# Kernel tuning notes

Measured on AMD Instinct MI355X. Metric: run time of the kernel, lower is better.

## Reference

```python
import jax, jax.numpy as jnp
import numpy as np

TOP_K = 2


def setup_inputs() -> dict:
    key = jax.random.key(0)
    ks = jax.random.split(key, 5)
    T, D, F, E = 1024, 1024, 2048, 16
    scale_d = 1.0 / np.sqrt(D)
    scale_f = 1.0 / np.sqrt(F)
    return {
        "x_TD": jax.random.normal(ks[0], (T, D), jnp.float32),
        "router_w_DE": jax.random.normal(ks[1], (D, E), jnp.float32) * scale_d,
        "kernel_gating_EDF": jax.random.normal(ks[2], (E, D, F), jnp.float32) * scale_d,
        "kernel_up_EDF": jax.random.normal(ks[3], (E, D, F), jnp.float32) * scale_d,
        "kernel_down_EFD": jax.random.normal(ks[4], (E, F, D), jnp.float32) * scale_f,
    }


def _router(x_TD, router_w_DE):
    # linear router -> softmax -> top-k, renormalized weights
    logits_TE = x_TD @ router_w_DE
    probs_TE = jax.nn.softmax(logits_TE, axis=-1)
    weights_TX, indices_TX = jax.lax.top_k(probs_TE, TOP_K)
    weights_TX = weights_TX / jnp.sum(weights_TX, axis=-1, keepdims=True)
    return weights_TX, indices_TX


def reference(x_TD, router_w_DE, kernel_gating_EDF, kernel_up_EDF, kernel_down_EFD):
    E = kernel_gating_EDF.shape[0]
    weights_TX, indices_TX = _router(x_TD, router_w_DE)
    # scatter top-k weights into a dense (T, E) combine matrix via one-hot
    one_hot_TXE = jax.nn.one_hot(indices_TX, E, dtype=x_TD.dtype)
    full_weights_TE = jnp.sum(one_hot_TXE * weights_TX[..., None], axis=1)
    # dense all-experts MoE (as in _moe_fwd)
    gating_TEF = jnp.einsum("TD,EDF->TEF", x_TD, kernel_gating_EDF)
    up_TEF = jnp.einsum("TD,EDF->TEF", x_TD, kernel_up_EDF)
    fuse_TEF = jax.nn.silu(gating_TEF) * up_TEF
    down_TED = jnp.einsum("TEF,EFD->TED", fuse_TEF, kernel_down_EFD)
    out_TD = jnp.einsum("TED,TE->TD", down_TED, full_weights_TE)
    return out_TD.astype(x_TD.dtype)
```

## Files before the change

kernel.cpp:

```cpp
#include <hip/hip_runtime.h>
#include <hip/hip_bf16.h>

typedef __bf16 bf16_t;
typedef __bf16 bf16x8 __attribute__((ext_vector_type(8)));
typedef __bf16 bf16x4 __attribute__((ext_vector_type(4)));
typedef float  f32x4  __attribute__((ext_vector_type(4)));

#define T_TOK 1024
#define DDIM  1024
#define FDIM  2048
#define NEXP  16
#define MAXR  192

#define WS_ENTRY_OFF   1024
#define WS_ENTRYW_OFF  66560
#define WS_XG_OFF      132096
#define WS_PART_OFF    132096
#define WS_FUSE_OFF    8520704

#define GLL16(g, l) __builtin_amdgcn_global_load_lds(                      \
    (const __attribute__((address_space(1))) unsigned int*)(g),            \
    (__attribute__((address_space(3))) unsigned int*)(l), 16, 0, 0)

#define FENCE()   asm volatile("" ::: "memory")
#define WAITVM(N) asm volatile("s_waitcnt vmcnt(" #N ")" ::: "memory")
#define WAITLG()  asm volatile("s_waitcnt lgkmcnt(0)" ::: "memory")
#define SCHEDB()  __builtin_amdgcn_sched_barrier(0)
#define SBAR()    __builtin_amdgcn_s_barrier()

__global__ __launch_bounds__(64) void router_kernel(
    const float* __restrict__ x, const float* __restrict__ rw,
    int* __restrict__ cnt, int* __restrict__ entry, float* __restrict__ entry_w)
{
    const int t = blockIdx.x;
    const int lane = threadIdx.x;
    float acc[NEXP];
#pragma unroll
    for (int e = 0; e < NEXP; ++e) acc[e] = 0.f;
#pragma unroll
    for (int i = 0; i < DDIM / 64; ++i) {
        const int d = lane + i * 64;
        const float xv = x[(size_t)t * DDIM + d];
        const float* r = rw + (size_t)d * NEXP;
#pragma unroll
        for (int e = 0; e < NEXP; ++e) acc[e] += xv * r[e];
    }
#pragma unroll
    for (int e = 0; e < NEXP; ++e) {
        float v = acc[e];
        for (int off = 32; off > 0; off >>= 1) v += __shfl_down(v, off);
        acc[e] = v;
    }
    if (lane == 0) {
        int i0 = -1, i1 = -1;
        float v0 = -1e30f, v1 = -1e30f;
#pragma unroll
        for (int e = 0; e < NEXP; ++e) {
            const float v = acc[e];
            if (v > v0)      { v1 = v0; i1 = i0; v0 = v; i0 = e; }
            else if (v > v1) { v1 = v;  i1 = e; }
        }
        const float e1 = __expf(v1 - v0);
        const float w0 = 1.f / (1.f + e1);
        const float w1 = e1 / (1.f + e1);
        int p = atomicAdd(&cnt[i0], 1);
        entry[i0 * T_TOK + p] = t * 2 + 0;
        entry_w[i0 * T_TOK + p] = w0;
        p = atomicAdd(&cnt[i1], 1);
        entry[i1 * T_TOK + p] = t * 2 + 1;
        entry_w[i1 * T_TOK + p] = w1;
    }
}

__global__ __launch_bounds__(256) void gather_kernel(
    const float* __restrict__ x, const int* __restrict__ cnt,
    const int* __restrict__ entry, bf16_t* __restrict__ xg)
{
    const int e  = blockIdx.x;
    const int i0 = blockIdx.y * 4;
    const int tid = threadIdx.x;
    int n_tok = cnt[e]; if (n_tok > MAXR) n_tok = MAXR;
#pragma unroll
    for (int rr = 0; rr < 4; ++rr) {
        const int i = i0 + rr;
        bf16x4 v4;
        v4[0] = (bf16_t)0.f; v4[1] = (bf16_t)0.f; v4[2] = (bf16_t)0.f; v4[3] = (bf16_t)0.f;
        if (i < n_tok) {
            const int tok = entry[e * T_TOK + i] >> 1;
            const float4 v = *(const float4*)(x + (size_t)tok * DDIM + tid * 4);
            v4[0] = (bf16_t)v.x; v4[1] = (bf16_t)v.y; v4[2] = (bf16_t)v.z; v4[3] = (bf16_t)v.w;
        }
        *(bf16x4*)(xg + ((size_t)e * MAXR + i) * DDIM + tid * 4) = v4;
    }
}

__global__ __launch_bounds__(256, 2) void ffn1_kernel(
    const bf16_t* __restrict__ xg,
    const float* __restrict__ wg, const float* __restrict__ wu,
    const int* __restrict__ cnt, const int* __restrict__ entry,
    bf16_t* __restrict__ fuse)
{
    const int e  = blockIdx.x;
    const int f0 = blockIdx.y * 64;
    int n_tok = cnt[e]; if (n_tok > MAXR) n_tok = MAXR;

    __shared__ __align__(16) bf16_t As[2][MAXR][32];
    __shared__ __align__(16) bf16_t Bgs[2][64][40];
    __shared__ __align__(16) bf16_t Bus[2][64][40];
    __shared__ int sem[MAXR];

    const int tid  = threadIdx.x;
    const int wave = tid >> 6;
    const int lane = tid & 63;
    const int r    = lane & 15;
    const int q    = lane >> 4;
    const int arow = lane >> 2;
    const int slot = (lane & 3) ^ (arow & 3);

    const bf16_t* xg_e = xg + (size_t)e * MAXR * DDIM;
    const float* wg_p = wg + (size_t)e * DDIM * FDIM + (size_t)(wave * 8) * FDIM + f0 + lane;
    const float* wu_p = wu + (size_t)e * DDIM * FDIM + (size_t)(wave * 8) * FDIM + f0 + lane;

    if (tid < MAXR) sem[tid] = (tid < n_tok) ? entry[e * T_TOK + tid] : -1;

    float rg[8], ru[8];
#pragma unroll
    for (int j = 0; j < 8; ++j) { rg[j] = wg_p[(size_t)j * FDIM]; ru[j] = wu_p[(size_t)j * FDIM]; }
    FENCE();
#pragma unroll
    for (int c = 0; c < 3; ++c) {
        const int rowb = wave * 48 + c * 16;
        const bf16_t* g = xg_e + (size_t)(rowb + arow) * DDIM + slot * 8;
        GLL16(g, &As[0][rowb][0] + lane * 8);
    }
    FENCE();
    WAITVM(3);
    {
        bf16x8 pg, pu;
#pragma unroll
        for (int j = 0; j < 8; ++j) { pg[j] = (bf16_t)rg[j]; pu[j] = (bf16_t)ru[j]; }
        *(bf16x8*)&Bgs[0][lane][wave * 8] = pg;
        *(bf16x8*)&Bus[0][lane][wave * 8] = pu;
    }
    wg_p += (size_t)32 * FDIM; wu_p += (size_t)32 * FDIM;
#pragma unroll
    for (int j = 0; j < 8; ++j) { rg[j] = wg_p[(size_t)j * FDIM]; ru[j] = wu_p[(size_t)j * FDIM]; }
    FENCE();
#pragma unroll
    for (int c = 0; c < 3; ++c) {
        const int rowb = wave * 48 + c * 16;
        const bf16_t* g = xg_e + (size_t)(rowb + arow) * DDIM + 32 + slot * 8;
        GLL16(g, &As[1][rowb][0] + lane * 8);
    }
    FENCE();
    WAITLG();
    SBAR();

    f32x4 accg[3][4], accu[3][4];
#pragma unroll
    for (int a = 0; a < 3; ++a)
#pragma unroll
        for (int b = 0; b < 4; ++b) {
            accg[a][b] = (f32x4){0.f, 0.f, 0.f, 0.f};
            accu[a][b] = (f32x4){0.f, 0.f, 0.f, 0.f};
        }

    for (int t = 0; t < 32; ++t) {
        const int cur = t & 1;
        if (t == 31) { WAITVM(0); } else { WAITVM(19); }
        SCHEDB();
        bf16x8 af[3], bg[4], bu[4];
#pragma unroll
        for (int mt = 0; mt < 3; ++mt) {
            const int m = wave * 48 + mt * 16 + r;
            af[mt] = *(const bf16x8*)&As[cur][m][(q ^ (r & 3)) * 8];
        }
#pragma unroll
        for (int nt = 0; nt < 4; ++nt) {
            bg[nt] = *(const bf16x8*)&Bgs[cur][nt * 16 + r][q * 8];
            bu[nt] = *(const bf16x8*)&Bus[cur][nt * 16 + r][q * 8];
        }
        if (t < 31) {
            WAITVM(3);
            bf16x8 pg, pu;
#pragma unroll
            for (int j = 0; j < 8; ++j) { pg[j] = (bf16_t)rg[j]; pu[j] = (bf16_t)ru[j]; }
            *(bf16x8*)&Bgs[cur ^ 1][lane][wave * 8] = pg;
            *(bf16x8*)&Bus[cur ^ 1][lane][wave * 8] = pu;
        }
        WAITLG();
        SCHEDB();
        if (t < 30) {
            wg_p += (size_t)32 * FDIM; wu_p += (size_t)32 * FDIM;
#pragma unroll
            for (int j = 0; j < 8; ++j) { rg[j] = wg_p[(size_t)j * FDIM]; ru[j] = wu_p[(size_t)j * FDIM]; }
            FENCE();
            const int kk = (t + 2) * 32;
#pragma unroll
            for (int c = 0; c < 3; ++c) {
                const int rowb = wave * 48 + c * 16;
                const bf16_t* g = xg_e + (size_t)(rowb + arow) * DDIM + kk + slot * 8;
                GLL16(g, &As[cur][rowb][0] + lane * 8);
            }
            FENCE();
        }
        __builtin_amdgcn_s_setprio(1);
#pragma unroll
        for (int mt = 0; mt < 3; ++mt)
#pragma unroll
            for (int nt = 0; nt < 4; ++nt) {
                accg[mt][nt] = __builtin_amdgcn_mfma_f32_16x16x32_bf16(af[mt], bg[nt], accg[mt][nt], 0, 0, 0);
                accu[mt][nt] = __builtin_amdgcn_mfma_f32_16x16x32_bf16(af[mt], bu[nt], accu[mt][nt], 0, 0, 0);
            }
        __builtin_amdgcn_s_setprio(0);
        SBAR();
    }

    bf16_t* fuse_e = fuse + (size_t)e * MAXR * FDIM + f0;
#pragma unroll
    for (int mt = 0; mt < 3; ++mt) {
#pragma unroll
        for (int j = 0; j < 4; ++j) {
            const int m = wave * 48 + mt * 16 + q * 4 + j;
            const bool valid = sem[m] >= 0;
            bf16_t* dst = fuse_e + (size_t)m * FDIM;
#pragma unroll
            for (int nt = 0; nt < 4; ++nt) {
                const float g = accg[mt][nt][j];
                const float u = accu[mt][nt][j];
                const float h = valid ? (g / (1.f + __expf(-g))) * u : 0.f;
                dst[nt * 16 + r] = (bf16_t)h;
            }
        }
    }
}

__global__ __launch_bounds__(256, 2) void ffn2_kernel(
    const bf16_t* __restrict__ fuse, const float* __restrict__ wd,
    const int* __restrict__ cnt, const int* __restrict__ entry,
    const float* __restrict__ entry_w, float* __restrict__ partial)
{
    const int e  = blockIdx.x;
    const int d0 = blockIdx.y * 32;
    int n_tok = cnt[e]; if (n_tok > MAXR) n_tok = MAXR;

    __shared__ __align__(16) bf16_t As[2][2][MAXR][32];
    __shared__ __align__(16) bf16_t Bs[2][32][72];
    __shared__ int   sem[MAXR];
    __shared__ float sw[MAXR];

    const int tid  = threadIdx.x;
    const int wave = tid >> 6;
    const int lane = tid & 63;
    const int r    = lane & 15;
    const int q    = lane >> 4;
    const int arow = lane >> 2;
    const int slot = (lane & 3) ^ (arow & 3);

    const bf16_t* fu_e = fuse + (size_t)e * MAXR * FDIM;
    const int bn = tid & 31;
    const int k8 = (tid >> 5) * 8;
    const float* wd_p = wd + (size_t)e * FDIM * DDIM + (size_t)k8 * DDIM + d0 + bn;

    if (tid < MAXR) {
        sem[tid] = (tid < n_tok) ? entry[e * T_TOK + tid] : -1;
        sw[tid]  = (tid < n_tok) ? entry_w[e * T_TOK + tid] : 0.f;
    }

    float rb[8];
#pragma unroll
    for (int j = 0; j < 8; ++j) rb[j] = wd_p[(size_t)j * DDIM];
    FENCE();
#pragma unroll
    for (int ks = 0; ks < 2; ++ks)
#pragma unroll
        for (int c = 0; c < 3; ++c) {
            const int rowb = wave * 48 + c * 16;
            const bf16_t* g = fu_e + (size_t)(rowb + arow) * FDIM + ks * 32 + slot * 8;
            GLL16(g, &As[0][ks][rowb][0] + lane * 8);
        }
    FENCE();
    WAITVM(6);
    {
        bf16x8 pb;
#pragma unroll
        for (int j = 0; j < 8; ++j) pb[j] = (bf16_t)rb[j];
        *(bf16x8*)&Bs[0][bn][k8] = pb;
    }
    wd_p += (size_t)64 * DDIM;
#pragma unroll
    for (int j = 0; j < 8; ++j) rb[j] = wd_p[(size_t)j * DDIM];
    FENCE();
#pragma unroll
    for (int ks = 0; ks < 2; ++ks)
#pragma unroll
        for (int c = 0; c < 3; ++c) {
            const int rowb = wave * 48 + c * 16;
            const bf16_t* g = fu_e + (size_t)(rowb + arow) * FDIM + 64 + ks * 32 + slot * 8;
            GLL16(g, &As[1][ks][rowb][0] + lane * 8);
        }
    FENCE();
    WAITLG();
    SBAR();

    f32x4 acc[3][2];
#pragma unroll
    for (int a = 0; a < 3; ++a)
#pragma unroll
        for (int b = 0; b < 2; ++b) acc[a][b] = (f32x4){0.f, 0.f, 0.f, 0.f};

    for (int t = 0; t < 32; ++t) {
        const int cur = t & 1;
        if (t == 31) { WAITVM(0); } else { WAITVM(14); }
        SCHEDB();
        bf16x8 af2[2][3], bb2[2][2];
#pragma unroll
        for (int ks = 0; ks < 2; ++ks) {
#pragma unroll
            for (int mt = 0; mt < 3; ++mt) {
                const int m = wave * 48 + mt * 16 + r;
                af2[ks][mt] = *(const bf16x8*)&As[cur][ks][m][(q ^ (r & 3)) * 8];
            }
#pragma unroll
            for (int nt = 0; nt < 2; ++nt)
                bb2[ks][nt] = *(const bf16x8*)&Bs[cur][nt * 16 + r][ks * 32 + q * 8];
        }
        if (t < 31) {
            WAITVM(6);
            bf16x8 pb;
#pragma unroll
            for (int j = 0; j < 8; ++j) pb[j] = (bf16_t)rb[j];
            *(bf16x8*)&Bs[cur ^ 1][bn][k8] = pb;
        }
        WAITLG();
        SCHEDB();
        if (t < 30) {
            wd_p += (size_t)64 * DDIM;
#pragma unroll
            for (int j = 0; j < 8; ++j) rb[j] = wd_p[(size_t)j * DDIM];
            FENCE();
            const int kk = (t + 2) * 64;
#pragma unroll
            for (int ks = 0; ks < 2; ++ks)
#pragma unroll
                for (int c = 0; c < 3; ++c) {
                    const int rowb = wave * 48 + c * 16;
                    const bf16_t* g = fu_e + (size_t)(rowb + arow) * FDIM + kk + ks * 32 + slot * 8;
                    GLL16(g, &As[cur][ks][rowb][0] + lane * 8);
                }
            FENCE();
        }
        __builtin_amdgcn_s_setprio(1);
#pragma unroll
        for (int ks = 0; ks < 2; ++ks)
#pragma unroll
            for (int mt = 0; mt < 3; ++mt)
#pragma unroll
                for (int nt = 0; nt < 2; ++nt)
                    acc[mt][nt] = __builtin_amdgcn_mfma_f32_16x16x32_bf16(af2[ks][mt], bb2[ks][nt], acc[mt][nt], 0, 0, 0);
        __builtin_amdgcn_s_setprio(0);
        SBAR();
    }

#pragma unroll
    for (int mt = 0; mt < 3; ++mt) {
#pragma unroll
        for (int j = 0; j < 4; ++j) {
            const int m = wave * 48 + mt * 16 + q * 4 + j;
            const int em = sem[m];
            if (em < 0) continue;
            const int t = em >> 1;
            const int sl = em & 1;
            const float w = sw[m];
            float* dst = partial + ((size_t)sl * T_TOK + t) * DDIM + d0;
#pragma unroll
            for (int nt = 0; nt < 2; ++nt)
                dst[nt * 16 + r] = acc[mt][nt][j] * w;
        }
    }
}

__global__ __launch_bounds__(256) void add_kernel(
    const float* __restrict__ partial, float* __restrict__ out)
{
    const int i = blockIdx.x * blockDim.x + threadIdx.x;
    const float4 a = ((const float4*)partial)[i];
    const float4 b = ((const float4*)(partial + (size_t)T_TOK * DDIM))[i];
    float4 o;
    o.x = a.x + b.x; o.y = a.y + b.y; o.z = a.z + b.z; o.w = a.w + b.w;
    ((float4*)out)[i] = o;
}

extern "C" void kernel_launch(void* const* d_in, const int* in_sizes, int n_in,
                              void* d_out, int out_size, void* d_ws, size_t ws_size,
                              hipStream_t stream) {
    const float* x  = (const float*)d_in[0];
    const float* rw = (const float*)d_in[1];
    const float* wg = (const float*)d_in[2];
    const float* wu = (const float*)d_in[3];
    const float* wd = (const float*)d_in[4];
    float* out = (float*)d_out;

    char* ws = (char*)d_ws;
    int*    cnt     = (int*)ws;
    int*    entry   = (int*)(ws + WS_ENTRY_OFF);
    float*  entry_w = (float*)(ws + WS_ENTRYW_OFF);
    bf16_t* xg      = (bf16_t*)(ws + WS_XG_OFF);
    float*  partial = (float*)(ws + WS_PART_OFF);
    bf16_t* fuse    = (bf16_t*)(ws + WS_FUSE_OFF);

    hipMemsetAsync(cnt, 0, 64, stream);

    router_kernel<<<T_TOK, 64, 0, stream>>>(x, rw, cnt, entry, entry_w);

    gather_kernel<<<dim3(NEXP, MAXR / 4), 256, 0, stream>>>(x, cnt, entry, xg);

    ffn1_kernel<<<dim3(NEXP, FDIM / 64), 256, 0, stream>>>(
        xg, wg, wu, cnt, entry, fuse);

    ffn2_kernel<<<dim3(NEXP, DDIM / 32), 256, 0, stream>>>(
        fuse, wd, cnt, entry, entry_w, partial);

    add_kernel<<<(T_TOK * DDIM / 4) / 256, 256, 0, stream>>>(partial, out);
}
```

Before: 432.5 us.

## Halve FFN tile widths for more blocks and stage router weights in LDS

```diff
diff --git a/kernel.cpp b/kernel.cpp
--- a/kernel.cpp
+++ b/kernel.cpp
@@ -4,6 +4,7 @@
 typedef __bf16 bf16_t;
 typedef __bf16 bf16x8 __attribute__((ext_vector_type(8)));
 typedef __bf16 bf16x4 __attribute__((ext_vector_type(4)));
+typedef __bf16 bf16x2 __attribute__((ext_vector_type(2)));
 typedef float  f32x4  __attribute__((ext_vector_type(4)));
 
 #define T_TOK 1024
@@ -28,22 +29,45 @@
 #define SCHEDB()  __builtin_amdgcn_sched_barrier(0)
 #define SBAR()    __builtin_amdgcn_s_barrier()
 
-__global__ __launch_bounds__(64) void router_kernel(
+__global__ __launch_bounds__(256) void router_kernel(
     const float* __restrict__ x, const float* __restrict__ rw,
     int* __restrict__ cnt, int* __restrict__ entry, float* __restrict__ entry_w)
 {
-    const int t = blockIdx.x;
-    const int lane = threadIdx.x;
+    __shared__ float rws[256][20];
+    const int tid  = threadIdx.x;
+    const int wave = tid >> 6;
+    const int lane = tid & 63;
+    const int t    = blockIdx.x * 4 + wave;
+
     float acc[NEXP];
 #pragma unroll
     for (int e = 0; e < NEXP; ++e) acc[e] = 0.f;
-#pragma unroll
-    for (int i = 0; i < DDIM / 64; ++i) {
-        const int d = lane + i * 64;
-        const float xv = x[(size_t)t * DDIM + d];
-        const float* r = rw + (size_t)d * NEXP;
-#pragma unroll
-        for (int e = 0; e < NEXP; ++e) acc[e] += xv * r[e];
+
+    for (int tile = 0; tile < 4; ++tile) {
+        const int d0 = tile * 256;
+        {
+            const float4* src = (const float4*)(rw + (size_t)(d0 + tid) * NEXP);
+            float4 a = src[0], b = src[1], c = src[2], d = src[3];
+            *(float4*)&rws[tid][0]  = a;
+            *(float4*)&rws[tid][4]  = b;
+            *(float4*)&rws[tid][8]  = c;
+            *(float4*)&rws[tid][12] = d;
+        }
+        __syncthreads();
+#pragma unroll
+        for (int i = 0; i < 4; ++i) {
+            const int row = i * 64 + lane;
+            const float xv = x[(size_t)t * DDIM + d0 + row];
+#pragma unroll
+            for (int e4 = 0; e4 < 4; ++e4) {
+                const float4 rv = *(const float4*)&rws[row][e4 * 4];
+                acc[e4 * 4 + 0] += xv * rv.x;
+                acc[e4 * 4 + 1] += xv * rv.y;
+                acc[e4 * 4 + 2] += xv * rv.z;
+                acc[e4 * 4 + 3] += xv * rv.w;
+            }
+        }
+        __syncthreads();
     }
 #pragma unroll
     for (int e = 0; e < NEXP; ++e) {
@@ -94,19 +118,19 @@
     }
 }
 
-__global__ __launch_bounds__(256, 2) void ffn1_kernel(
+__global__ __launch_bounds__(256, 4) void ffn1_kernel(
     const bf16_t* __restrict__ xg,
     const float* __restrict__ wg, const float* __restrict__ wu,
     const int* __restrict__ cnt, const int* __restrict__ entry,
     bf16_t* __restrict__ fuse)
 {
     const int e  = blockIdx.x;
-    const int f0 = blockIdx.y * 64;
+    const int f0 = blockIdx.y * 32;
     int n_tok = cnt[e]; if (n_tok > MAXR) n_tok = MAXR;
 
     __shared__ __align__(16) bf16_t As[2][MAXR][32];
-    __shared__ __align__(16) bf16_t Bgs[2][64][40];
-    __shared__ __align__(16) bf16_t Bus[2][64][40];
+    __shared__ __align__(16) bf16_t Bgs[2][32][40];
+    __shared__ __align__(16) bf16_t Bus[2][32][40];
     __shared__ int sem[MAXR];
 
     const int tid  = threadIdx.x;
@@ -116,16 +140,18 @@
     const int q    = lane >> 4;
     const int arow = lane >> 2;
     const int slot = (lane & 3) ^ (arow & 3);
+    const int bcol = lane & 31;
+    const int brow0 = wave * 8 + ((lane >> 5) << 2);
 
     const bf16_t* xg_e = xg + (size_t)e * MAXR * DDIM;
-    const float* wg_p = wg + (size_t)e * DDIM * FDIM + (size_t)(wave * 8) * FDIM + f0 + lane;
-    const float* wu_p = wu + (size_t)e * DDIM * FDIM + (size_t)(wave * 8) * FDIM + f0 + lane;
+    const float* wg_p = wg + (size_t)e * DDIM * FDIM + (size_t)brow0 * FDIM + f0 + bcol;
+    const float* wu_p = wu + (size_t)e * DDIM * FDIM + (size_t)brow0 * FDIM + f0 + bcol;
 
     if (tid < MAXR) sem[tid] = (tid < n_tok) ? entry[e * T_TOK + tid] : -1;
 
-    float rg[8], ru[8];
-#pragma unroll
-    for (int j = 0; j < 8; ++j) { rg[j] = wg_p[(size_t)j * FDIM]; ru[j] = wu_p[(size_t)j * FDIM]; }
+    float rg[4], ru[4];
+#pragma unroll
+    for (int j = 0; j < 4; ++j) { rg[j] = wg_p[(size_t)j * FDIM]; ru[j] = wu_p[(size_t)j * FDIM]; }
     FENCE();
 #pragma unroll
     for (int c = 0; c < 3; ++c) {
@@ -136,15 +162,15 @@
     FENCE();
     WAITVM(3);
     {
-        bf16x8 pg, pu;
-#pragma unroll
-        for (int j = 0; j < 8; ++j) { pg[j] = (bf16_t)rg[j]; pu[j] = (bf16_t)ru[j]; }
-        *(bf16x8*)&Bgs[0][lane][wave * 8] = pg;
-        *(bf16x8*)&Bus[0][lane][wave * 8] = pu;
+        bf16x4 pg, pu;
+#pragma unroll
+        for (int j = 0; j < 4; ++j) { pg[j] = (bf16_t)rg[j]; pu[j] = (bf16_t)ru[j]; }
+        *(bf16x4*)&Bgs[0][bcol][brow0] = pg;
+        *(bf16x4*)&Bus[0][bcol][brow0] = pu;
     }
     wg_p += (size_t)32 * FDIM; wu_p += (size_t)32 * FDIM;
 #pragma unroll
-    for (int j = 0; j < 8; ++j) { rg[j] = wg_p[(size_t)j * FDIM]; ru[j] = wu_p[(size_t)j * FDIM]; }
+    for (int j = 0; j < 4; ++j) { rg[j] = wg_p[(size_t)j * FDIM]; ru[j] = wu_p[(size_t)j * FDIM]; }
     FENCE();
 #pragma unroll
     for (int c = 0; c < 3; ++c) {
@@ -156,44 +182,44 @@
     WAITLG();
     SBAR();
 
-    f32x4 accg[3][4], accu[3][4];
+    f32x4 accg[3][2], accu[3][2];
 #pragma unroll
     for (int a = 0; a < 3; ++a)
 #pragma unroll
-        for (int b = 0; b < 4; ++b) {
+        for (int b = 0; b < 2; ++b) {
             accg[a][b] = (f32x4){0.f, 0.f, 0.f, 0.f};
             accu[a][b] = (f32x4){0.f, 0.f, 0.f, 0.f};
         }
 
     for (int t = 0; t < 32; ++t) {
         const int cur = t & 1;
-        if (t == 31) { WAITVM(0); } else { WAITVM(19); }
+        if (t == 31) { WAITVM(0); } else { WAITVM(11); }
         SCHEDB();
-        bf16x8 af[3], bg[4], bu[4];
+        bf16x8 af[3], bg[2], bu[2];
 #pragma unroll
         for (int mt = 0; mt < 3; ++mt) {
             const int m = wave * 48 + mt * 16 + r;
             af[mt] = *(const bf16x8*)&As[cur][m][(q ^ (r & 3)) * 8];
         }
 #pragma unroll
-        for (int nt = 0; nt < 4; ++nt) {
+        for (int nt = 0; nt < 2; ++nt) {
             bg[nt] = *(const bf16x8*)&Bgs[cur][nt * 16 + r][q * 8];
             bu[nt] = *(const bf16x8*)&Bus[cur][nt * 16 + r][q * 8];
         }
         if (t < 31) {
             WAITVM(3);
-            bf16x8 pg, pu;
-#pragma unroll
-            for (int j = 0; j < 8; ++j) { pg[j] = (bf16_t)rg[j]; pu[j] = (bf16_t)ru[j]; }
-            *(bf16x8*)&Bgs[cur ^ 1][lane][wave * 8] = pg;
-            *(bf16x8*)&Bus[cur ^ 1][lane][wave * 8] = pu;
+            bf16x4 pg, pu;
+#pragma unroll
+            for (int j = 0; j < 4; ++j) { pg[j] = (bf16_t)rg[j]; pu[j] = (bf16_t)ru[j]; }
+            *(bf16x4*)&Bgs[cur ^ 1][bcol][brow0] = pg;
+            *(bf16x4*)&Bus[cur ^ 1][bcol][brow0] = pu;
         }
         WAITLG();
         SCHEDB();
         if (t < 30) {
             wg_p += (size_t)32 * FDIM; wu_p += (size_t)32 * FDIM;
 #pragma unroll
-            for (int j = 0; j < 8; ++j) { rg[j] = wg_p[(size_t)j * FDIM]; ru[j] = wu_p[(size_t)j * FDIM]; }
+            for (int j = 0; j < 4; ++j) { rg[j] = wg_p[(size_t)j * FDIM]; ru[j] = wu_p[(size_t)j * FDIM]; }
             FENCE();
             const int kk = (t + 2) * 32;
 #pragma unroll
@@ -208,7 +234,7 @@
 #pragma unroll
         for (int mt = 0; mt < 3; ++mt)
 #pragma unroll
-            for (int nt = 0; nt < 4; ++nt) {
+            for (int nt = 0; nt < 2; ++nt) {
                 accg[mt][nt] = __builtin_amdgcn_mfma_f32_16x16x32_bf16(af[mt], bg[nt], accg[mt][nt], 0, 0, 0);
                 accu[mt][nt] = __builtin_amdgcn_mfma_f32_16x16x32_bf16(af[mt], bu[nt], accu[mt][nt], 0, 0, 0);
             }
@@ -225,7 +251,7 @@
             const bool valid = sem[m] >= 0;
             bf16_t* dst = fuse_e + (size_t)m * FDIM;
 #pragma unroll
-            for (int nt = 0; nt < 4; ++nt) {
+            for (int nt = 0; nt < 2; ++nt) {
                 const float g = accg[mt][nt][j];
                 const float u = accu[mt][nt][j];
                 const float h = valid ? (g / (1.f + __expf(-g))) * u : 0.f;
@@ -235,17 +261,17 @@
     }
 }
 
-__global__ __launch_bounds__(256, 2) void ffn2_kernel(
+__global__ __launch_bounds__(256, 4) void ffn2_kernel(
     const bf16_t* __restrict__ fuse, const float* __restrict__ wd,
     const int* __restrict__ cnt, const int* __restrict__ entry,
     const float* __restrict__ entry_w, float* __restrict__ partial)
 {
     const int e  = blockIdx.x;
-    const int d0 = blockIdx.y * 32;
+    const int d0 = blockIdx.y * 16;
     int n_tok = cnt[e]; if (n_tok > MAXR) n_tok = MAXR;
 
-    __shared__ __align__(16) bf16_t As[2][2][MAXR][32];
-    __shared__ __align__(16) bf16_t Bs[2][32][72];
+    __shared__ __align__(16) bf16_t As[2][MAXR][32];
+    __shared__ __align__(16) bf16_t Bs[2][16][40];
     __shared__ int   sem[MAXR];
     __shared__ float sw[MAXR];
 
@@ -256,108 +282,89 @@
     const int q    = lane >> 4;
     const int arow = lane >> 2;
     const int slot = (lane & 3) ^ (arow & 3);
+    const int bcol = lane & 15;
+    const int brow0 = wave * 8 + ((lane >> 4) << 1);
 
     const bf16_t* fu_e = fuse + (size_t)e * MAXR * FDIM;
-    const int bn = tid & 31;
-    const int k8 = (tid >> 5) * 8;
-    const float* wd_p = wd + (size_t)e * FDIM * DDIM + (size_t)k8 * DDIM + d0 + bn;
+    const float* wd_p = wd + (size_t)e * FDIM * DDIM + (size_t)brow0 * DDIM + d0 + bcol;
 
     if (tid < MAXR) {
         sem[tid] = (tid < n_tok) ? entry[e * T_TOK + tid] : -1;
         sw[tid]  = (tid < n_tok) ? entry_w[e * T_TOK + tid] : 0.f;
     }
 
-    float rb[8];
-#pragma unroll
-    for (int j = 0; j < 8; ++j) rb[j] = wd_p[(size_t)j * DDIM];
-    FENCE();
-#pragma unroll
-    for (int ks = 0; ks < 2; ++ks)
-#pragma unroll
-        for (int c = 0; c < 3; ++c) {
-            const int rowb = wave * 48 + c * 16;
-            const bf16_t* g = fu_e + (size_t)(rowb + arow) * FDIM + ks * 32 + slot * 8;
-            GLL16(g, &As[0][ks][rowb][0] + lane * 8);
-        }
-    FENCE();
-    WAITVM(6);
+    float rb[2];
+#pragma unroll
+    for (int j = 0; j < 2; ++j) rb[j] = wd_p[(size_t)j * DDIM];
+    FENCE();
+#pragma unroll
+    for (int c = 0; c < 3; ++c) {
+        const int rowb = wave * 48 + c * 16;
+        const bf16_t* g = fu_e + (size_t)(rowb + arow) * FDIM + slot * 8;
+        GLL16(g, &As[0][rowb][0] + lane * 8);
+    }
+    FENCE();
+    WAITVM(3);
     {
-        bf16x8 pb;
-#pragma unroll
-        for (int j = 0; j < 8; ++j) pb[j] = (bf16_t)rb[j];
-        *(bf16x8*)&Bs[0][bn][k8] = pb;
-    }
-    wd_p += (size_t)64 * DDIM;
-#pragma unroll
-    for (int j = 0; j < 8; ++j) rb[j] = wd_p[(size_t)j * DDIM];
-    FENCE();
-#pragma unroll
-    for (int ks = 0; ks < 2; ++ks)
-#pragma unroll
-        for (int c = 0; c < 3; ++c) {
-            const int rowb = wave * 48 + c * 16;
-            const bf16_t* g = fu_e + (size_t)(rowb + arow) * FDIM + 64 + ks * 32 + slot * 8;
-            GLL16(g, &As[1][ks][rowb][0] + lane * 8);
-        }
+        bf16x2 pb;
+        pb[0] = (bf16_t)rb[0]; pb[1] = (bf16_t)rb[1];
+        *(bf16x2*)&Bs[0][bcol][brow0] = pb;
+    }
+    wd_p += (size_t)32 * DDIM;
+#pragma unroll
+    for (int j = 0; j < 2; ++j) rb[j] = wd_p[(size_t)j * DDIM];
+    FENCE();
+#pragma unroll
+    for (int c = 0; c < 3; ++c) {
+        const int rowb = wave * 48 + c * 16;
+        const bf16_t* g = fu_e + (size_t)(rowb + arow) * FDIM + 32 + slot * 8;
+        GLL16(g, &As[1][rowb][0] + lane * 8);
+    }
     FENCE();
     WAITLG();
     SBAR();
 
-    f32x4 acc[3][2];
-#pragma unroll
-    for (int a = 0; a < 3; ++a)
-#pragma unroll
-        for (int b = 0; b < 2; ++b) acc[a][b] = (f32x4){0.f, 0.f, 0.f, 0.f};
-
-    for (int t = 0; t < 32; ++t) {
+    f32x4 acc[3];
+#pragma unroll
+    for (int a = 0; a < 3; ++a) acc[a] = (f32x4){0.f, 0.f, 0.f, 0.f};
+
+    for (int t = 0; t < 64; ++t) {
         const int cur = t & 1;
-        if (t == 31) { WAITVM(0); } else { WAITVM(14); }
+        if (t == 63) { WAITVM(0); } else { WAITVM(5); }
         SCHEDB();
-        bf16x8 af2[2][3], bb2[2][2];
-#pragma unroll
-        for (int ks = 0; ks < 2; ++ks) {
-#pragma unroll
-            for (int mt = 0; mt < 3; ++mt) {
-                const int m = wave * 48 + mt * 16 + r;
-                af2[ks][mt] = *(const bf16x8*)&As[cur][ks][m][(q ^ (r & 3)) * 8];
-            }
-#pragma unroll
-            for (int nt = 0; nt < 2; ++nt)
-                bb2[ks][nt] = *(const bf16x8*)&Bs[cur][nt * 16 + r][ks * 32 + q * 8];
-        }
-        if (t < 31) {
-            WAITVM(6);
-            bf16x8 pb;
-#pragma unroll
-            for (int j = 0; j < 8; ++j) pb[j] = (bf16_t)rb[j];
-            *(bf16x8*)&Bs[cur ^ 1][bn][k8] = pb;
+        bf16x8 af[3], bb;
+#pragma unroll
+        for (int mt = 0; mt < 3; ++mt) {
+            const int m = wave * 48 + mt * 16 + r;
+            af[mt] = *(const bf16x8*)&As[cur][m][(q ^ (r & 3)) * 8];
+        }
+        bb = *(const bf16x8*)&Bs[cur][r][q * 8];
+        if (t < 63) {
+            WAITVM(3);
+            bf16x2 pb;
+            pb[0] = (bf16_t)rb[0]; pb[1] = (bf16_t)rb[1];
+            *(bf16x2*)&Bs[cur ^ 1][bcol][brow0] = pb;
         }
         WAITLG();
         SCHEDB();
-        if (t < 30) {
-            wd_p += (size_t)64 * DDIM;
-#pragma unroll
-            for (int j = 0; j < 8; ++j) rb[j] = wd_p[(size_t)j * DDIM];
+        if (t < 62) {
+            wd_p += (size_t)32 * DDIM;
+#pragma unroll
+            for (int j = 0; j < 2; ++j) rb[j] = wd_p[(size_t)j * DDIM];
             FENCE();
-            const int kk = (t + 2) * 64;
-#pragma unroll
-            for (int ks = 0; ks < 2; ++ks)
-#pragma unroll
-                for (int c = 0; c < 3; ++c) {
-                    const int rowb = wave * 48 + c * 16;
-                    const bf16_t* g = fu_e + (size_t)(rowb + arow) * FDIM + kk + ks * 32 + slot * 8;
-                    GLL16(g, &As[cur][ks][rowb][0] + lane * 8);
-                }
+            const int kk = (t + 2) * 32;
+#pragma unroll
+            for (int c = 0; c < 3; ++c) {
+                const int rowb = wave * 48 + c * 16;
+                const bf16_t* g = fu_e + (size_t)(rowb + arow) * FDIM + kk + slot * 8;
+                GLL16(g, &As[cur][rowb][0] + lane * 8);
+            }
             FENCE();
         }
         __builtin_amdgcn_s_setprio(1);
 #pragma unroll
-        for (int ks = 0; ks < 2; ++ks)
-#pragma unroll
-            for (int mt = 0; mt < 3; ++mt)
-#pragma unroll
-                for (int nt = 0; nt < 2; ++nt)
-                    acc[mt][nt] = __builtin_amdgcn_mfma_f32_16x16x32_bf16(af2[ks][mt], bb2[ks][nt], acc[mt][nt], 0, 0, 0);
+        for (int mt = 0; mt < 3; ++mt)
+            acc[mt] = __builtin_amdgcn_mfma_f32_16x16x32_bf16(af[mt], bb, acc[mt], 0, 0, 0);
         __builtin_amdgcn_s_setprio(0);
         SBAR();
     }
@@ -373,9 +380,7 @@
             const int sl = em & 1;
             const float w = sw[m];
             float* dst = partial + ((size_t)sl * T_TOK + t) * DDIM + d0;
-#pragma unroll
-            for (int nt = 0; nt < 2; ++nt)
-                dst[nt * 16 + r] = acc[mt][nt][j] * w;
+            dst[r] = acc[mt][j] * w;
         }
     }
 }
@@ -411,14 +416,14 @@
 
     hipMemsetAsync(cnt, 0, 64, stream);
 
-    router_kernel<<<T_TOK, 64, 0, stream>>>(x, rw, cnt, entry, entry_w);
+    router_kernel<<<T_TOK / 4, 256, 0, stream>>>(x, rw, cnt, entry, entry_w);
 
     gather_kernel<<<dim3(NEXP, MAXR / 4), 256, 0, stream>>>(x, cnt, entry, xg);
 
-    ffn1_kernel<<<dim3(NEXP, FDIM / 64), 256, 0, stream>>>(
+    ffn1_kernel<<<dim3(NEXP, FDIM / 32), 256, 0, stream>>>(
         xg, wg, wu, cnt, entry, fuse);
 
-    ffn2_kernel<<<dim3(NEXP, DDIM / 32), 256, 0, stream>>>(
+    ffn2_kernel<<<dim3(NEXP, DDIM / 16), 256, 0, stream>>>(
         fuse, wd, cnt, entry, entry_w, partial);
 
     add_kernel<<<(T_TOK * DDIM / 4) / 256, 256, 0, stream>>>(partial, out);
```

Measured after the change: 520.1 us. 20.2% more time.
